# Optimization experiments

Hardware: AMD Instinct MI355X
Metric: run time of the kernel (lower is better)

Reference implementation:

```python
import jax, jax.numpy as jnp
import numpy as np

N, E, F_IN, F_E, L = 10000, 50000, 40, 10, 64

def setup_inputs() -> dict:
    key = jax.random.key(0)
    ks = jax.random.split(key, 12)
    f32 = jnp.float32
    def rn(k, shape, s=0.1):
        return jax.random.normal(k, shape, dtype=f32) * s
    return {
        "x": rn(ks[0], (N, F_IN), 1.0),
        "edge_index": jax.random.randint(ks[1], (2, E), 0, N),
        "edge_attr": rn(ks[2], (E, F_E), 1.0),
        "lin0_w": rn(ks[3], (F_IN, L)), "lin0_b": jnp.zeros((L,), f32),
        "nn1_w": rn(ks[4], (F_E, L)), "nn1_b": jnp.zeros((L,), f32),
        "nn2_w": rn(ks[5], (L, L * L), 0.02), "nn2_b": jnp.zeros((L * L,), f32),
        "conv_root": rn(ks[6], (L, L)), "conv_bias": jnp.zeros((L,), f32),
        "gru_w_ih": rn(ks[7], (L, 3 * L)), "gru_w_hh": rn(ks[8], (L, 3 * L)),
        "gru_b_ih": jnp.zeros((3 * L,), f32), "gru_b_hh": jnp.zeros((3 * L,), f32),
        "lin1_w": rn(ks[9], (L, L)), "lin1_b": jnp.zeros((L,), f32),
        "lin2_w": rn(ks[10], (L, 1)), "lin2_b": jnp.zeros((1,), f32),
    }

def reference(x, edge_index, edge_attr, lin0_w, lin0_b, nn1_w, nn1_b,
              nn2_w, nn2_b, conv_root, conv_bias, gru_w_ih, gru_w_hh,
              gru_b_ih, gru_b_hh, lin1_w, lin1_b, lin2_w, lin2_b):
    n = x.shape[0]
    l = lin0_b.shape[0]
    src, dst = edge_index[0], edge_index[1]

    # mean-aggregation normalization (nodes with no in-edges -> 0)
    deg = jax.ops.segment_sum(jnp.ones_like(edge_attr[:, 0]), dst, num_segments=n)
    inv_deg = (1.0 / jnp.maximum(deg, 1.0))[:, None]  # [N,1]

    # edge-conditioned weights: nnet(edge_attr).view(E, L, L) -- edge_attr is
    # loop-invariant so compute once (same math as recomputing each iter)
    w_edge = (jax.nn.relu(edge_attr @ nn1_w + nn1_b) @ nn2_w + nn2_b).reshape(-1, l, l)

    out = jax.nn.relu(x @ lin0_w + lin0_b)  # [N,L]
    h = out
    for _ in range(3):
        # NNConv: gather src feats, per-edge matvec, scatter-mean, + root + bias
        msg = jnp.einsum('ei,eio->eo', out[src], w_edge)  # [E,L]
        agg = jax.ops.segment_sum(msg, dst, num_segments=n) * inv_deg
        m = jax.nn.relu(agg + out @ conv_root + conv_bias)
        # single-step GRU (torch nn.GRU equations)
        gi = m @ gru_w_ih + gru_b_ih
        gh = h @ gru_w_hh + gru_b_hh
        r = jax.nn.sigmoid(gi[:, :l] + gh[:, :l])
        z = jax.nn.sigmoid(gi[:, l:2 * l] + gh[:, l:2 * l])
        ng = jnp.tanh(gi[:, 2 * l:] + r * gh[:, 2 * l:])
        h = (1.0 - z) * ng + z * h
        out = h

    out = jax.nn.relu(out @ lin1_w + lin1_b)
    return out @ lin2_w + lin2_b  # [N,1]
```

## Files before the change

kernel.cpp:

```cpp
#include <hip/hip_runtime.h>
#include <hip/hip_bf16.h>

#define NN 10000
#define NP 10240
#define NE 50000
#define FIN 40
#define FE 10
#define MCH 20

typedef float f32x4 __attribute__((ext_vector_type(4)));
typedef short s16x8 __attribute__((ext_vector_type(8)));

__device__ __forceinline__ float bcast(float v, int lane) {
    return __uint_as_float(__builtin_amdgcn_readlane(__float_as_uint(v), lane));
}
__device__ __forceinline__ int bcast_i(int v, int lane) {
    return __builtin_amdgcn_readlane(v, lane);
}
__device__ __forceinline__ ushort f2bf(float f) {
    uint u = __float_as_uint(f);
    uint r = (u + 0x7FFFu + ((u >> 16) & 1u)) >> 16;
    return (ushort)r;
}
__device__ __forceinline__ float bf2f(ushort h) {
    return __uint_as_float(((uint)h) << 16);
}

__global__ void k_count(const int* __restrict__ ei, int* __restrict__ deg) {
    int e = blockIdx.x * 256 + threadIdx.x;
    if (e < NE) atomicAdd(&deg[ei[NE + e]], 1);
}

__global__ __launch_bounds__(1024) void k_scan(const int* __restrict__ deg,
                                               int* __restrict__ rowp,
                                               int* __restrict__ fill,
                                               float* __restrict__ invd) {
    __shared__ int wsum[16];
    __shared__ int chunkbase;
    int tid = threadIdx.x, lane = tid & 63, wv = tid >> 6;
    if (tid == 0) chunkbase = 0;
    __syncthreads();
    for (int base = 0; base < NN; base += 1024) {
        int idx = base + tid;
        int v = (idx < NN) ? deg[idx] : 0;
        int s = v;
#pragma unroll
        for (int off = 1; off < 64; off <<= 1) {
            int t = __shfl_up(s, off, 64);
            if (lane >= off) s += t;
        }
        if (lane == 63) wsum[wv] = s;
        __syncthreads();
        int carry = chunkbase;
        if (wv == 0 && lane < 16) {
            int x = wsum[lane];
#pragma unroll
            for (int off = 1; off < 16; off <<= 1) {
                int t = __shfl_up(x, off, 64);
                if (lane >= off) x += t;
            }
            wsum[lane] = x;
        }
        __syncthreads();
        int wpre = (wv == 0) ? 0 : wsum[wv - 1];
        int incl = carry + wpre + s;
        if (idx < NN) {
            rowp[idx] = incl - v;
            fill[idx] = incl - v;
            invd[idx] = 1.0f / (float)(v > 0 ? v : 1);
        }
        __syncthreads();
        if (tid == 0) chunkbase = carry + wsum[15];
        __syncthreads();
    }
    if (tid == 0) rowp[NN] = NE;
}

__global__ void k_fill(const int* __restrict__ ei, int* __restrict__ fill,
                       int* __restrict__ csrs, int* __restrict__ csre) {
    int e = blockIdx.x * 256 + threadIdx.x;
    if (e < NE) {
        int d = ei[NE + e];
        int p = atomicAdd(&fill[d], 1);
        csrs[p] = ei[e];
        csre[p] = e;
    }
}

__global__ __launch_bounds__(256) void k_w2f(const float* __restrict__ n2w,
                                             ushort* __restrict__ W2FH,
                                             ushort* __restrict__ W2FL) {
    int lane = threadIdx.x & 63, wvl = threadIdx.x >> 6;
    int ki = blockIdx.x * 4 + wvl;
    float v = n2w[(size_t)ki * 64 + lane];
    ushort hi = f2bf(v);
    ushort lo = f2bf(v - bf2f(hi));
    W2FH[(size_t)lane * 4096 + ki] = hi;
    W2FL[(size_t)lane * 4096 + ki] = lo;
}

__global__ __launch_bounds__(256) void k_edge_h(const float* __restrict__ ea,
                                                const float* __restrict__ w1,
                                                const float* __restrict__ b1,
                                                float* __restrict__ hE) {
    int lane = threadIdx.x & 63, wv = threadIdx.x >> 6;
    int e = blockIdx.x * 4 + wv;
    float av = (lane < FE) ? ea[e * FE + lane] : 0.f;
    float acc = b1[lane];
#pragma unroll
    for (int j = 0; j < FE; ++j) acc += bcast(av, j) * w1[j * 64 + lane];
    hE[e * 64 + lane] = fmaxf(acc, 0.f);
}

__global__ __launch_bounds__(256) void k_lin0(const float* __restrict__ x,
                                              const float* __restrict__ w0,
                                              const float* __restrict__ b0,
                                              float* __restrict__ F) {
    int lane = threadIdx.x & 63, wv = threadIdx.x >> 6;
    int n = blockIdx.x * 4 + wv;
    float xv = (lane < FIN) ? x[n * FIN + lane] : 0.f;
    float acc = b0[lane];
#pragma unroll
    for (int k = 0; k < FIN; ++k) acc += bcast(xv, k) * w0[k * 64 + lane];
    F[n * 64 + lane] = fmaxf(acc, 0.f);
}

__global__ __launch_bounds__(256) void k_gather(
    const float* __restrict__ F, const float* __restrict__ hE,
    const int* __restrict__ rowp, const int* __restrict__ csrs,
    const int* __restrict__ csre,
    ushort* __restrict__ GH, float* __restrict__ Usb) {
    int tid = threadIdx.x, lane = tid & 63, wv = tid >> 6;
    int n = __builtin_amdgcn_readfirstlane(blockIdx.x * 4 + wv);
    int beg = __builtin_amdgcn_readfirstlane(rowp[n]);
    int end = __builtin_amdgcn_readfirstlane(rowp[n + 1]);

    float G[64];
#pragma unroll
    for (int k = 0; k < 64; ++k) G[k] = 0.f;
    float usum = 0.f;
    {
        int p0 = beg + lane;
        int sl = (p0 < end) ? csrs[p0] : 0;
        int el = (p0 < end) ? csre[p0] : 0;
        int nb = min(end - beg, 64);
        for (int j = 0; j < nb; ++j) {
            int s = bcast_i(sl, j);
            int e = bcast_i(el, j);
            float u = F[(size_t)s * 64 + lane];
            float hv = hE[(size_t)e * 64 + lane];
            usum += u;
#pragma unroll
            for (int k = 0; k < 64; ++k) G[k] = fmaf(bcast(hv, k), u, G[k]);
        }
        for (int p = beg + 64; p < end; ++p) {
            int s = __builtin_amdgcn_readfirstlane(csrs[p]);
            int e = __builtin_amdgcn_readfirstlane(csre[p]);
            float u = F[(size_t)s * 64 + lane];
            float hv = hE[(size_t)e * 64 + lane];
            usum += u;
#pragma unroll
            for (int k = 0; k < 64; ++k) G[k] = fmaf(bcast(hv, k), u, G[k]);
        }
    }
    Usb[(size_t)n * 64 + lane] = usum;
    ushort* gout = GH + (size_t)n * 4096 + lane;
#pragma unroll
    for (int k = 0; k < 64; ++k) gout[k * 64] = f2bf(G[k]);
}

__global__ __launch_bounds__(512) void k_contract(
    const ushort* __restrict__ GH, const ushort* __restrict__ W2FH,
    const ushort* __restrict__ W2FL, float* __restrict__ AggP) {
    __shared__ __align__(16) ushort BH[64 * 264];
    __shared__ __align__(16) ushort BL[64 * 264];
    int tid = threadIdx.x, lane = tid & 63, wv = tid >> 6;
    int ks = blockIdx.x & 15;
    int mc = blockIdx.x >> 4;
    int kbase = ks * 256;
    int otile = wv & 3, mhalf = wv >> 2;
    int arow = lane & 15, agrp = lane >> 4;
    int o = otile * 16 + arow;

#pragma unroll
    for (int rep = 0; rep < 4; ++rep) {
        int off = rep * 4096 + tid * 8;
        int row = off >> 8, col = off & 255;
        *(s16x8*)&BH[row * 264 + col] =
            *(const s16x8*)&W2FH[(size_t)row * 4096 + kbase + col];
        *(s16x8*)&BL[row * 264 + col] =
            *(const s16x8*)&W2FL[(size_t)row * 4096 + kbase + col];
    }
    __syncthreads();

    int mg0 = mc * MCH;
    int mgend = mg0 + MCH;
    float* ap = AggP + (size_t)ks * NN * 64;
    for (int mg = mg0 + mhalf * 2; mg < mgend; mg += 4) {
        const ushort* pA = GH + (size_t)(mg * 16 + arow) * 4096 + kbase;
        const ushort* pB = GH + (size_t)((mg + 1) * 16 + arow) * 4096 + kbase;
        f32x4 a0h = {0.f, 0.f, 0.f, 0.f};
        f32x4 a0l = {0.f, 0.f, 0.f, 0.f};
        f32x4 a1h = {0.f, 0.f, 0.f, 0.f};
        f32x4 a1l = {0.f, 0.f, 0.f, 0.f};
#pragma unroll 4
        for (int s = 0; s < 8; ++s) {
            int kil = s * 32 + agrp * 8;
            s16x8 a0 = *(const s16x8*)&pA[kil];
            s16x8 a1 = *(const s16x8*)&pB[kil];
            s16x8 bh = *(const s16x8*)&BH[o * 264 + kil];
            s16x8 bl = *(const s16x8*)&BL[o * 264 + kil];
            a0h = __builtin_amdgcn_mfma_f32_16x16x32_bf16(a0, bh, a0h, 0, 0, 0);
            a1h = __builtin_amdgcn_mfma_f32_16x16x32_bf16(a1, bh, a1h, 0, 0, 0);
            a0l = __builtin_amdgcn_mfma_f32_16x16x32_bf16(a0, bl, a0l, 0, 0, 0);
            a1l = __builtin_amdgcn_mfma_f32_16x16x32_bf16(a1, bl, a1l, 0, 0, 0);
        }
        f32x4 acc0 = a0h + a0l;
        f32x4 acc1 = a1h + a1l;
#pragma unroll
        for (int r = 0; r < 4; ++r) {
            int n0r = mg * 16 + agrp * 4 + r;
            if (n0r < NN) ap[(size_t)n0r * 64 + o] = acc0[r];
            int n1r = (mg + 1) * 16 + agrp * 4 + r;
            if (n1r < NN) ap[(size_t)n1r * 64 + o] = acc1[r];
        }
    }
}

__global__ __launch_bounds__(256) void k_epi(
    const float* __restrict__ AggP, const float* __restrict__ Usb,
    const float* __restrict__ B2, const float* __restrict__ invd,
    const float* __restrict__ F, const float* __restrict__ Wroot,
    const float* __restrict__ broot, const float* __restrict__ Wih,
    const float* __restrict__ Whh, const float* __restrict__ bih,
    const float* __restrict__ bhh, float* __restrict__ Fout) {
    int lane = threadIdx.x & 63, wv = threadIdx.x >> 6;
    int nq = blockIdx.x * 16 + wv * 4;

    float fv[4], uv[4], aa[4], rt[4], bt[4];
#pragma unroll
    for (int q = 0; q < 4; ++q) {
        size_t idx = (size_t)(nq + q) * 64 + lane;
        fv[q] = F[idx];
        uv[q] = Usb[idx];
        float s = 0.f;
#pragma unroll
        for (int ks = 0; ks < 16; ++ks) s += AggP[(size_t)ks * NN * 64 + idx];
        aa[q] = s;
        rt[q] = broot[lane];
        bt[q] = 0.f;
    }
#pragma unroll 8
    for (int k = 0; k < 64; ++k) {
        float wr = Wroot[k * 64 + lane];
        float b2 = B2[k * 64 + lane];
#pragma unroll
        for (int q = 0; q < 4; ++q) {
            rt[q] = fmaf(bcast(fv[q], k), wr, rt[q]);
            bt[q] = fmaf(bcast(uv[q], k), b2, bt[q]);
        }
    }
    float m[4];
#pragma unroll
    for (int q = 0; q < 4; ++q)
        m[q] = fmaxf((aa[q] + bt[q]) * invd[nq + q] + rt[q], 0.f);

    float sr[4], sz[4], gn[4], gh[4];
#pragma unroll
    for (int q = 0; q < 4; ++q) {
        sr[q] = bih[lane] + bhh[lane];
        sz[q] = bih[64 + lane] + bhh[64 + lane];
        gn[q] = bih[128 + lane];
        gh[q] = bhh[128 + lane];
    }
#pragma unroll 8
    for (int k = 0; k < 64; ++k) {
        float wi0 = Wih[k * 192 + lane];
        float wi1 = Wih[k * 192 + 64 + lane];
        float wi2 = Wih[k * 192 + 128 + lane];
        float wh0 = Whh[k * 192 + lane];
        float wh1 = Whh[k * 192 + 64 + lane];
        float wh2 = Whh[k * 192 + 128 + lane];
#pragma unroll
        for (int q = 0; q < 4; ++q) {
            float mk = bcast(m[q], k), hk = bcast(fv[q], k);
            sr[q] = fmaf(mk, wi0, fmaf(hk, wh0, sr[q]));
            sz[q] = fmaf(mk, wi1, fmaf(hk, wh1, sz[q]));
            gn[q] = fmaf(mk, wi2, gn[q]);
            gh[q] = fmaf(hk, wh2, gh[q]);
        }
    }
#pragma unroll
    for (int q = 0; q < 4; ++q) {
        float rr = 1.f / (1.f + __expf(-sr[q]));
        float zz = 1.f / (1.f + __expf(-sz[q]));
        float ng = tanhf(gn[q] + rr * gh[q]);
        Fout[(size_t)(nq + q) * 64 + lane] = (1.f - zz) * ng + zz * fv[q];
    }
}

__global__ __launch_bounds__(256) void k_final(const float* __restrict__ F,
                                               const float* __restrict__ W1,
                                               const float* __restrict__ b1f,
                                               const float* __restrict__ W2l,
                                               const float* __restrict__ b2f,
                                               float* __restrict__ out) {
    int lane = threadIdx.x & 63, wv = threadIdx.x >> 6;
    int n = blockIdx.x * 4 + wv;
    float fv = F[n * 64 + lane];
    float acc = b1f[lane];
#pragma unroll
    for (int k = 0; k < 64; ++k) acc += bcast(fv, k) * W1[k * 64 + lane];
    acc = fmaxf(acc, 0.f);
    float p = acc * W2l[lane];
#pragma unroll
    for (int off = 32; off; off >>= 1) p += __shfl_xor(p, off, 64);
    if (lane == 0) out[n] = p + b2f[0];
}

extern "C" void kernel_launch(void* const* d_in, const int* in_sizes, int n_in,
                              void* d_out, int out_size, void* d_ws, size_t ws_size,
                              hipStream_t stream) {
    const float* x = (const float*)d_in[0];
    const int* ei = (const int*)d_in[1];
    const float* ea = (const float*)d_in[2];
    const float* l0w = (const float*)d_in[3];
    const float* l0b = (const float*)d_in[4];
    const float* n1w = (const float*)d_in[5];
    const float* n1b = (const float*)d_in[6];
    const float* n2w = (const float*)d_in[7];
    const float* n2b = (const float*)d_in[8];
    const float* cr = (const float*)d_in[9];
    const float* cb = (const float*)d_in[10];
    const float* wih = (const float*)d_in[11];
    const float* whh = (const float*)d_in[12];
    const float* bih = (const float*)d_in[13];
    const float* bhh = (const float*)d_in[14];
    const float* l1w = (const float*)d_in[15];
    const float* l1b = (const float*)d_in[16];
    const float* l2w = (const float*)d_in[17];
    const float* l2b = (const float*)d_in[18];

    char* w = (char*)d_ws;
    size_t off = 0;
    float* F0 = (float*)(w + off); off += (size_t)NN * 64 * 4;
    float* F1 = (float*)(w + off); off += (size_t)NN * 64 * 4;
    float* hE = (float*)(w + off); off += (size_t)NE * 64 * 4;
    ushort* W2FH = (ushort*)(w + off); off += (size_t)64 * 4096 * 2;
    ushort* W2FL = (ushort*)(w + off); off += (size_t)64 * 4096 * 2;
    ushort* GH = (ushort*)(w + off); off += (size_t)NP * 4096 * 2;
    float* AggP = (float*)(w + off); off += (size_t)16 * NN * 64 * 4;
    float* Usb = (float*)(w + off); off += (size_t)NN * 64 * 4;
    float* invd = (float*)(w + off); off += (size_t)NN * 4;
    int* deg = (int*)(w + off); off += (size_t)NN * 4;
    int* rowp = (int*)(w + off); off += (size_t)(NN + 1) * 4 + 252; off &= ~(size_t)255;
    int* fill = (int*)(w + off); off += (size_t)NN * 4;
    int* csrs = (int*)(w + off); off += (size_t)NE * 4;
    int* csre = (int*)(w + off); off += (size_t)NE * 4;

    hipMemsetAsync(deg, 0, NN * 4, stream);
    k_count<<<(NE + 255) / 256, 256, 0, stream>>>(ei, deg);
    k_scan<<<1, 1024, 0, stream>>>(deg, rowp, fill, invd);
    k_fill<<<(NE + 255) / 256, 256, 0, stream>>>(ei, fill, csrs, csre);
    k_w2f<<<1024, 256, 0, stream>>>(n2w, W2FH, W2FL);
    k_edge_h<<<NE / 4, 256, 0, stream>>>(ea, n1w, n1b, hE);
    k_lin0<<<NN / 4, 256, 0, stream>>>(x, l0w, l0b, F0);
    float* Fcur = F0;
    float* Fnxt = F1;
    for (int it = 0; it < 3; ++it) {
        k_gather<<<NN / 4, 256, 0, stream>>>(Fcur, hE, rowp, csrs, csre, GH, Usb);
        k_contract<<<512, 512, 0, stream>>>(GH, W2FH, W2FL, AggP);
        k_epi<<<NN / 16, 256, 0, stream>>>(AggP, Usb, n2b, invd, Fcur, cr, cb,
                                           wih, whh, bih, bhh, Fnxt);
        float* t = Fcur; Fcur = Fnxt; Fnxt = t;
    }
    k_final<<<NN / 4, 256, 0, stream>>>(Fcur, l1w, l1b, l2w, l2b, (float*)d_out);
}
```

Before: 334.7 us.

## Store gathered G matrix in MFMA-tiled layout via LDS staging

The gather kernel now stages each node's 64x64 bf16 G tile in shared memory and writes it to global memory in a 16-row tiled, chunk-interleaved layout using 16-byte vector stores. The old version wrote scattered 2-byte stores. The contract kernel reads A fragments from this layout, so each MFMA operand load for 16 rows becomes contiguous instead of strided across 8KB rows. The cost is 32KB of LDS per gather block, which may reduce occupancy, plus an extra barrier.

```diff
diff --git a/kernel.cpp b/kernel.cpp
--- a/kernel.cpp
+++ b/kernel.cpp
@@ -129,7 +129,8 @@
     const float* __restrict__ F, const float* __restrict__ hE,
     const int* __restrict__ rowp, const int* __restrict__ csrs,
     const int* __restrict__ csre,
-    ushort* __restrict__ GH, float* __restrict__ Usb) {
+    ushort* __restrict__ GHT, float* __restrict__ Usb) {
+    __shared__ __align__(16) ushort Gs[4][4096];
     int tid = threadIdx.x, lane = tid & 63, wv = tid >> 6;
     int n = __builtin_amdgcn_readfirstlane(blockIdx.x * 4 + wv);
     int beg = __builtin_amdgcn_readfirstlane(rowp[n]);
@@ -164,13 +165,20 @@
         }
     }
     Usb[(size_t)n * 64 + lane] = usum;
-    ushort* gout = GH + (size_t)n * 4096 + lane;
-#pragma unroll
-    for (int k = 0; k < 64; ++k) gout[k * 64] = f2bf(G[k]);
+#pragma unroll
+    for (int k = 0; k < 64; ++k) Gs[wv][k * 64 + lane] = f2bf(G[k]);
+    __syncthreads();
+    int r = n & 15;
+    ushort* gout = GHT + (size_t)(n >> 4) * 65536 + r * 8;
+#pragma unroll
+    for (int it = 0; it < 8; ++it) {
+        int kc = it * 64 + lane;
+        *(s16x8*)&gout[(size_t)kc * 128] = *(const s16x8*)&Gs[wv][kc * 8];
+    }
 }
 
 __global__ __launch_bounds__(512) void k_contract(
-    const ushort* __restrict__ GH, const ushort* __restrict__ W2FH,
+    const ushort* __restrict__ GHT, const ushort* __restrict__ W2FH,
     const ushort* __restrict__ W2FL, float* __restrict__ AggP) {
     __shared__ __align__(16) ushort BH[64 * 264];
     __shared__ __align__(16) ushort BL[64 * 264];
@@ -197,17 +205,18 @@
     int mgend = mg0 + MCH;
     float* ap = AggP + (size_t)ks * NN * 64;
     for (int mg = mg0 + mhalf * 2; mg < mgend; mg += 4) {
-        const ushort* pA = GH + (size_t)(mg * 16 + arow) * 4096 + kbase;
-        const ushort* pB = GH + (size_t)((mg + 1) * 16 + arow) * 4096 + kbase;
+        const ushort* pA = GHT + (size_t)mg * 65536 + (size_t)ks * 4096 + arow * 8;
+        const ushort* pB = pA + 65536;
         f32x4 a0h = {0.f, 0.f, 0.f, 0.f};
         f32x4 a0l = {0.f, 0.f, 0.f, 0.f};
         f32x4 a1h = {0.f, 0.f, 0.f, 0.f};
         f32x4 a1l = {0.f, 0.f, 0.f, 0.f};
 #pragma unroll 4
         for (int s = 0; s < 8; ++s) {
+            int aoff = (s * 4 + agrp) * 128;
             int kil = s * 32 + agrp * 8;
-            s16x8 a0 = *(const s16x8*)&pA[kil];
-            s16x8 a1 = *(const s16x8*)&pB[kil];
+            s16x8 a0 = *(const s16x8*)&pA[aoff];
+            s16x8 a1 = *(const s16x8*)&pB[aoff];
             s16x8 bh = *(const s16x8*)&BH[o * 264 + kil];
             s16x8 bl = *(const s16x8*)&BL[o * 264 + kil];
             a0h = __builtin_amdgcn_mfma_f32_16x16x32_bf16(a0, bh, a0h, 0, 0, 0);
@@ -348,7 +357,7 @@
     float* hE = (float*)(w + off); off += (size_t)NE * 64 * 4;
     ushort* W2FH = (ushort*)(w + off); off += (size_t)64 * 4096 * 2;
     ushort* W2FL = (ushort*)(w + off); off += (size_t)64 * 4096 * 2;
-    ushort* GH = (ushort*)(w + off); off += (size_t)NP * 4096 * 2;
+    ushort* GHT = (ushort*)(w + off); off += (size_t)NP * 4096 * 2;
     float* AggP = (float*)(w + off); off += (size_t)16 * NN * 64 * 4;
     float* Usb = (float*)(w + off); off += (size_t)NN * 64 * 4;
     float* invd = (float*)(w + off); off += (size_t)NN * 4;
@@ -368,8 +377,8 @@
     float* Fcur = F0;
     float* Fnxt = F1;
     for (int it = 0; it < 3; ++it) {
-        k_gather<<<NN / 4, 256, 0, stream>>>(Fcur, hE, rowp, csrs, csre, GH, Usb);
-        k_contract<<<512, 512, 0, stream>>>(GH, W2FH, W2FL, AggP);
+        k_gather<<<NN / 4, 256, 0, stream>>>(Fcur, hE, rowp, csrs, csre, GHT, Usb);
+        k_contract<<<512, 512, 0, stream>>>(GHT, W2FH, W2FL, AggP);
         k_epi<<<NN / 16, 256, 0, stream>>>(AggP, Usb, n2b, invd, Fcur, cr, cb,
                                            wih, whh, bih, bhh, Fnxt);
         float* t = Fcur; Fcur = Fnxt; Fnxt = t;
```

Result: faster. 323.8 us (-3.3%).
